# Performance work log

Hardware: AMD Instinct MI355X
Metric: run time of the kernel (lower is better)

Reference implementation:

```python
import jax, jax.numpy as jnp
import numpy as np

D, E, DFF, TOPK = 768, 4, 1024, 2


def setup_inputs() -> dict:
    key = jax.random.key(0)
    ks = jax.random.split(key, 6)
    s = 0.02  # init scale for weights
    return {
        "input_ids": jax.random.normal(ks[0], (8, 2048, D), dtype=jnp.float32),
        "W": jax.random.normal(ks[1], (D, D), dtype=jnp.float32) * s,
        "b": jnp.zeros((D,), dtype=jnp.float32),
        "Wg": jax.random.normal(ks[2], (D, E), dtype=jnp.float32) * s,
        "bg": jnp.zeros((E,), dtype=jnp.float32),
        "W1": jax.random.normal(ks[3], (E, D, DFF), dtype=jnp.float32) * s,
        "b1": jnp.zeros((E, DFF), dtype=jnp.float32),
        "W2": jax.random.normal(ks[4], (E, DFF, D), dtype=jnp.float32) * s,
        "b2": jnp.zeros((E, D), dtype=jnp.float32),
    }


def reference(input_ids, W, b, Wg, bg, W1, b1, W2, b2):
    B, S, _ = input_ids.shape
    # Dense projection feeding the MoE layer
    h = jnp.einsum("bsd,de->bse", input_ids, W) + b          # [B,S,D]
    t = h.reshape(-1, D)                                      # [T,D] tokens

    # Token-choice router: softmax over experts, top-2, renormalized gates
    logits = t @ Wg + bg                                      # [T,E]
    probs = jax.nn.softmax(logits, axis=-1)
    vals, idx = jax.lax.top_k(probs, TOPK)                    # [T,K]
    gates = vals / jnp.sum(vals, axis=-1, keepdims=True)
    # Dense combine weights [T,E]: zero for non-selected experts
    comb = jnp.sum(jax.nn.one_hot(idx, E, dtype=t.dtype) * gates[..., None], axis=1)

    # Expert FFNs (E small -> compute all experts, weighted combine)
    pre = jnp.einsum("td,edf->etf", t, W1) + b1[:, None, :]   # [E,T,DFF]
    y_e = jnp.einsum("etf,efd->etd", jax.nn.gelu(pre), W2) + b2[:, None, :]
    out = jnp.einsum("te,etd->td", comb, y_e)                 # [T,D]
    return out.reshape(B, S, D)
```

## Files before the change

kernel.cpp:

```cpp
#include <hip/hip_runtime.h>

#define DIM 768
#define NEXP 4
#define DFF_ 1024
#define CAP 16384

typedef __attribute__((ext_vector_type(4))) float f32x4;
typedef __attribute__((ext_vector_type(8))) short s16x8;

__device__ __forceinline__ unsigned short f32_to_bf16(float f) {
  unsigned int u = __float_as_uint(f);
  unsigned int r = (u + 0x7FFFu + ((u >> 16) & 1u)) >> 16;
  return (unsigned short)r;
}
__device__ __forceinline__ float bf16_to_f32(unsigned short u) {
  return __uint_as_float(((unsigned int)u) << 16);
}

__global__ void transpose_bf16_kernel(const float* __restrict__ in,
                                      unsigned short* __restrict__ out,
                                      int R, int C, int ldo, int zOut) {
  __shared__ float tile[32][33];
  const int bx = blockIdx.x, by = blockIdx.y, bz = blockIdx.z;
  in  += (size_t)bz * R * C;
  out += (size_t)bz * zOut;
  const int tx = threadIdx.x, ty = threadIdx.y;
#pragma unroll
  for (int i = 0; i < 4; i++) {
    int r = by * 32 + ty + i * 8;
    int c = bx * 32 + tx;
    tile[ty + i * 8][tx] = in[(size_t)r * C + c];
  }
  __syncthreads();
#pragma unroll
  for (int i = 0; i < 4; i++) {
    int oc = bx * 32 + ty + i * 8;
    int orow = by * 32 + tx;
    out[(size_t)oc * ldo + orow] = f32_to_bf16(tile[tx][ty + i * 8]);
  }
}

__global__ void wfg_kernel(const float* __restrict__ W, const float* __restrict__ Wg,
                           const float* __restrict__ b, const float* __restrict__ bg,
                           float* __restrict__ wfg, float* __restrict__ bgp) {
  int gid = blockIdx.x * 256 + threadIdx.x;
  if (gid < DIM * NEXP) {
    int k = gid >> 2, e = gid & 3;
    const float* wr = W + (size_t)k * DIM;
    float acc = 0.f;
    for (int d = 0; d < DIM; d++) acc += wr[d] * Wg[d * NEXP + e];
    wfg[gid] = acc;
  } else if (gid < DIM * NEXP + NEXP) {
    int e = gid - DIM * NEXP;
    float acc = bg[e];
    for (int d = 0; d < DIM; d++) acc += b[d] * Wg[d * NEXP + e];
    bgp[e] = acc;
  }
}

__global__ void router_kernel(const float* __restrict__ x, const float* __restrict__ wfg,
                              const float* __restrict__ bgp,
                              int2* __restrict__ rte, float2* __restrict__ rtg,
                              unsigned short* __restrict__ xbf) {
  __shared__ float wfgS[DIM * NEXP];
  const int tid = threadIdx.x;
  for (int i = tid; i < DIM * NEXP; i += 256) wfgS[i] = wfg[i];
  __syncthreads();
  const int w = tid >> 6, lane = tid & 63;
  const size_t t = (size_t)blockIdx.x * 4 + w;
  const float* xr = x + t * DIM;
  unsigned short* xbr = xbf + t * DIM;
  float a0 = 0.f, a1 = 0.f, a2 = 0.f, a3 = 0.f;
#pragma unroll
  for (int i = 0; i < 6; i++) {
    int k = i * 128 + lane * 2;
    float2 xv = *(const float2*)(xr + k);
    ushort2 pk;
    pk.x = f32_to_bf16(xv.x);
    pk.y = f32_to_bf16(xv.y);
    *(ushort2*)(xbr + k) = pk;
    a0 += xv.x * wfgS[k * 4 + 0] + xv.y * wfgS[k * 4 + 4];
    a1 += xv.x * wfgS[k * 4 + 1] + xv.y * wfgS[k * 4 + 5];
    a2 += xv.x * wfgS[k * 4 + 2] + xv.y * wfgS[k * 4 + 6];
    a3 += xv.x * wfgS[k * 4 + 3] + xv.y * wfgS[k * 4 + 7];
  }
#pragma unroll
  for (int off = 32; off > 0; off >>= 1) {
    a0 += __shfl_xor(a0, off);
    a1 += __shfl_xor(a1, off);
    a2 += __shfl_xor(a2, off);
    a3 += __shfl_xor(a3, off);
  }
  if (lane == 0) {
    float l[NEXP] = {a0 + bgp[0], a1 + bgp[1], a2 + bgp[2], a3 + bgp[3]};
    float m = fmaxf(fmaxf(l[0], l[1]), fmaxf(l[2], l[3]));
    float p[NEXP]; float s = 0.f;
#pragma unroll
    for (int e = 0; e < NEXP; e++) { p[e] = expf(l[e] - m); s += p[e]; }
#pragma unroll
    for (int e = 0; e < NEXP; e++) p[e] /= s;
    int i1 = 0;
#pragma unroll
    for (int e = 1; e < NEXP; e++) if (p[e] > p[i1]) i1 = e;
    int i2 = -1;
#pragma unroll
    for (int e = 0; e < NEXP; e++) { if (e == i1) continue; if (i2 < 0 || p[e] > p[i2]) i2 = e; }
    float denom = p[i1] + p[i2];
    rte[t] = make_int2(i1, i2);
    rtg[t] = make_float2(p[i1] / denom, p[i2] / denom);
  }
}

__global__ void assign_kernel(const int2* __restrict__ rte, const float2* __restrict__ rtg,
                              int* __restrict__ cnt, int* __restrict__ idx_tok,
                              float* __restrict__ gate_sel, int2* __restrict__ tok_slot) {
  __shared__ int hist[NEXP];
  __shared__ int base[NEXP];
  const int tid = threadIdx.x;
  if (tid < NEXP) hist[tid] = 0;
  __syncthreads();
  const int t = blockIdx.x * 256 + tid;
  int2 e = rte[t];
  float2 g = rtg[t];
  int r1 = atomicAdd(&hist[e.x], 1);
  int r2 = atomicAdd(&hist[e.y], 1);
  __syncthreads();
  if (tid < NEXP) base[tid] = atomicAdd(&cnt[tid], hist[tid]);
  __syncthreads();
  int s1 = base[e.x] + r1, s2 = base[e.y] + r2;
  idx_tok[e.x * CAP + s1] = t;  gate_sel[e.x * CAP + s1] = g.x;
  idx_tok[e.y * CAP + s2] = t;  gate_sel[e.y * CAP + s2] = g.y;
  tok_slot[t] = make_int2((e.x << 14) | s1, (e.y << 14) | s2);
}

__global__ void combine_kernel(const unsigned short* __restrict__ y,
                               const int2* __restrict__ tok_slot,
                               const float2* __restrict__ rtg,
                               const int* __restrict__ cnts,
                               const float* __restrict__ b2,
                               float* __restrict__ out) {
  __shared__ float b2S[NEXP * DIM];
  const int tid = threadIdx.x;
  for (int i = tid; i < NEXP * DIM; i += 256) b2S[i] = b2[i];
  const int t0 = (cnts[0] + 127) >> 7, t1 = (cnts[1] + 127) >> 7, t2 = (cnts[2] + 127) >> 7;
  const int rb[NEXP] = {0, t0 * 128, (t0 + t1) * 128, (t0 + t1 + t2) * 128};
  __syncthreads();
  const int w = tid >> 6, lane = tid & 63;
  const size_t t = (size_t)blockIdx.x * 4 + w;
  int2 v = tok_slot[t];
  float2 cg = rtg[t];
  const int e1 = v.x >> 14, s1 = v.x & (CAP - 1);
  const int e2 = v.y >> 14, s2 = v.y & (CAP - 1);
  const unsigned short* y1 = y + (size_t)(rb[e1] + s1) * DIM;
  const unsigned short* y2 = y + (size_t)(rb[e2] + s2) * DIM;
  float* op = out + t * DIM;
  const float* bp1 = b2S + e1 * DIM;
  const float* bp2 = b2S + e2 * DIM;
#pragma unroll
  for (int k = 0; k < 12; k++) {
    int n = k * 64 + lane;
    op[n] = bf16_to_f32(y1[n]) + bf16_to_f32(y2[n]) + cg.x * bp1[n] + cg.y * bp2[n];
  }
}

template <int MODE, int CH>
__launch_bounds__(256)
__global__ void gemm_kernel(const unsigned short* __restrict__ A, const int lda,
                            const unsigned short* __restrict__ Bt, const int ldb,
                            const int K, const int N,
                            const float* __restrict__ bias,
                            const int* __restrict__ idx_tok,
                            const float* __restrict__ gate_sel,
                            const int* __restrict__ cnts,
                            unsigned short* __restrict__ outB, const int ldo) {
  const int lin = blockIdx.y * gridDim.x + blockIdx.x;
  const int nT = gridDim.x;
  const int xcd = lin & 7, t8 = lin >> 3;
  int bn = 0, bm0 = 0;
  int bmLoc = 0, cnt = 1 << 30, segBase = 0, gRow0 = 0;

  if constexpr (MODE == 0) {
    const int perXcd = gridDim.y >> 3;
    const int mi = t8 % CH;
    const int rest = t8 / CH;
    bn = rest % nT;
    const int mc = rest / nT;
    bm0 = (xcd * perXcd + mc * CH + mi) * 128;
  } else {
    const int c0 = cnts[0], c1 = cnts[1], c2 = cnts[2], c3 = cnts[3];
    const int t0 = (c0 + 127) >> 7, t1 = (c1 + 127) >> 7,
              t2 = (c2 + 127) >> 7, t3 = (c3 + 127) >> 7;
    const int p1 = t0, p2 = p1 + t1, p3 = p2 + t2, tot = p3 + t3;
    const int perXcd = (tot + 7) >> 3;
    bn = t8 % nT;
    const int mloc = t8 / nT;
    if (mloc >= perXcd) return;
    const int mIdx = xcd * perXcd + mloc;
    if (mIdx >= tot) return;
    const int seg = (mIdx >= p2) ? ((mIdx >= p3) ? 3 : 2) : ((mIdx >= p1) ? 1 : 0);
    const int pre = (seg == 3) ? p3 : (seg == 2) ? p2 : (seg == 1) ? p1 : 0;
    bmLoc = (mIdx - pre) * 128;
    segBase = seg * CAP;
    gRow0 = mIdx * 128;
    cnt = (seg == 3) ? c3 : (seg == 2) ? c2 : (seg == 1) ? c1 : c0;
    Bt += (size_t)seg * N * ldb;
    if constexpr (MODE == 1) bias += (size_t)seg * N;
  }

  __shared__ unsigned short As[2][128 * 32];
  __shared__ unsigned short Bs[2][128 * 32];
  __shared__ int idxS[128];
  __shared__ float gateS[128];

  const int tid = threadIdx.x;
  const int w = tid >> 6;
  const int lane = tid & 63;

  if constexpr (MODE == 1) {
    if (tid < 128) {
      int r = bmLoc + tid;
      int cl = (r < cnt) ? r : bmLoc;
      idxS[tid] = idx_tok[segBase + cl];
      gateS[tid] = gate_sel[segBase + cl];
    }
    __syncthreads();
  }

  const int r0 = tid >> 2, r1 = 64 + r0;
  const int gq = (tid & 3) ^ (r0 & 3);
  const unsigned short *aP0, *aP1;
  if constexpr (MODE == 0) {
    aP0 = A + (size_t)(bm0 + r0) * lda + gq * 8;
    aP1 = A + (size_t)(bm0 + r1) * lda + gq * 8;
  } else if constexpr (MODE == 1) {
    aP0 = A + (size_t)idxS[r0] * lda + gq * 8;
    aP1 = A + (size_t)idxS[r1] * lda + gq * 8;
  } else {
    aP0 = A + (size_t)(gRow0 + r0) * lda + gq * 8;
    aP1 = A + (size_t)(gRow0 + r1) * lda + gq * 8;
  }
  const unsigned short* bP0 = Bt + (size_t)(bn * 128 + r0) * ldb + gq * 8;
  const unsigned short* bP1 = Bt + (size_t)(bn * 128 + r1) * ldb + gq * 8;

#define ISSUE(bufi, kk)                                                                        \
  {                                                                                            \
    char* la0 = (char*)As[bufi] + w * 1024;                                                    \
    char* la1 = (char*)As[bufi] + 4096 + w * 1024;                                             \
    char* lb0 = (char*)Bs[bufi] + w * 1024;                                                    \
    char* lb1 = (char*)Bs[bufi] + 4096 + w * 1024;                                             \
    __builtin_amdgcn_global_load_lds((const __attribute__((address_space(1))) void*)(aP0 + (kk)), \
                                     (__attribute__((address_space(3))) void*)la0, 16, 0, 0);  \
    __builtin_amdgcn_global_load_lds((const __attribute__((address_space(1))) void*)(aP1 + (kk)), \
                                     (__attribute__((address_space(3))) void*)la1, 16, 0, 0);  \
    __builtin_amdgcn_global_load_lds((const __attribute__((address_space(1))) void*)(bP0 + (kk)), \
                                     (__attribute__((address_space(3))) void*)lb0, 16, 0, 0);  \
    __builtin_amdgcn_global_load_lds((const __attribute__((address_space(1))) void*)(bP1 + (kk)), \
                                     (__attribute__((address_space(3))) void*)lb1, 16, 0, 0);  \
  }

  f32x4 acc[4][4];
#pragma unroll
  for (int i = 0; i < 4; i++)
#pragma unroll
    for (int j = 0; j < 4; j++) acc[i][j] = (f32x4){0.f, 0.f, 0.f, 0.f};

  const int quad = lane >> 4;
  const int m16 = lane & 15;
  const int wm = (w & 1) * 64;
  const int wn = (w >> 1) * 64;
  const int sw = (quad ^ (m16 & 3)) * 16;

  ISSUE(0, 0);
  int buf = 0;
  for (int k0 = 0; k0 < K; k0 += 32) {
    __syncthreads();
    if (k0 + 32 < K) ISSUE(buf ^ 1, k0 + 32);
    const char* Ab = (const char*)As[buf];
    const char* Bb = (const char*)Bs[buf];
    s16x8 af[4], bf4[4];
#pragma unroll
    for (int i = 0; i < 4; i++)
      af[i] = *(const s16x8*)(Ab + (wm + i * 16 + m16) * 64 + sw);
#pragma unroll
    for (int j = 0; j < 4; j++)
      bf4[j] = *(const s16x8*)(Bb + (wn + j * 16 + m16) * 64 + sw);
#pragma unroll
    for (int i = 0; i < 4; i++)
#pragma unroll
      for (int j = 0; j < 4; j++)
        acc[i][j] = __builtin_amdgcn_mfma_f32_16x16x32_bf16(af[i], bf4[j], acc[i][j], 0, 0, 0);
    buf ^= 1;
  }
#undef ISSUE

#pragma unroll
  for (int i = 0; i < 4; i++) {
    const int rloc = wm + i * 16 + quad * 4;
#pragma unroll
    for (int j = 0; j < 4; j++) {
      const int col = bn * 128 + wn + j * 16 + m16;
      if constexpr (MODE == 0) {
        float bv = bias[col];
#pragma unroll
        for (int r = 0; r < 4; r++)
          outB[(size_t)(bm0 + rloc + r) * ldo + col] = f32_to_bf16(acc[i][j][r] + bv);
      } else if constexpr (MODE == 1) {
        float bv = bias[col];
#pragma unroll
        for (int r = 0; r < 4; r++) {
          if (bmLoc + rloc + r < cnt) {
            float v = acc[i][j][r] + bv;
            float t3 = v + 0.044715f * v * v * v;
            float e2 = exp2f(t3 * 2.302208206984525f);
            float rc = __builtin_amdgcn_rcpf(1.0f + e2);
            float g = v - v * rc;
            outB[(size_t)(gRow0 + rloc + r) * ldo + col] = f32_to_bf16(g * gateS[rloc + r]);
          }
        }
      } else {
#pragma unroll
        for (int r = 0; r < 4; r++) {
          if (bmLoc + rloc + r < cnt)
            outB[(size_t)(gRow0 + rloc + r) * ldo + col] = f32_to_bf16(acc[i][j][r]);
        }
      }
    }
  }
}

extern "C" void kernel_launch(void* const* d_in, const int* in_sizes, int n_in,
                              void* d_out, int out_size, void* d_ws, size_t ws_size,
                              hipStream_t stream) {
  (void)in_sizes; (void)n_in; (void)out_size; (void)ws_size;
  const float* x  = (const float*)d_in[0];
  const float* W  = (const float*)d_in[1];
  const float* b  = (const float*)d_in[2];
  const float* Wg = (const float*)d_in[3];
  const float* bg = (const float*)d_in[4];
  const float* W1 = (const float*)d_in[5];
  const float* b1 = (const float*)d_in[6];
  const float* W2 = (const float*)d_in[7];
  const float* b2 = (const float*)d_in[8];
  float* out = (float*)d_out;
  char* ws = (char*)d_ws;

  unsigned short* tbf  = (unsigned short*)(ws + 0);
  unsigned short* w1t  = (unsigned short*)(ws + 25165824);
  unsigned short* w2t  = (unsigned short*)(ws + 31457280);
  float* wfg           = (float*)(ws + 37748736);
  float* bgp           = (float*)(ws + 37761024);
  int2*  rte           = (int2*)(ws + 37761280);
  float2* rtg          = (float2*)(ws + 37892352);
  int*   cnt           = (int*)(ws + 38023424);
  int*   idx_tok       = (int*)(ws + 38023680);
  float* gate_sel      = (float*)(ws + 38285824);
  int2*  tok_slot      = (int2*)(ws + 38547968);
  unsigned short* g    = (unsigned short*)(ws + 38679040);
  unsigned short* xbf  = (unsigned short*)(ws + 38679040);
  unsigned short* wt   = (unsigned short*)(ws + 63844864);
  unsigned short* y    = (unsigned short*)(ws + 106574336);

  hipMemsetAsync(cnt, 0, NEXP * sizeof(int), stream);
  transpose_bf16_kernel<<<dim3(24, 24, 1), dim3(32, 8), 0, stream>>>(W, wt, 768, 768, 768, 589824);
  transpose_bf16_kernel<<<dim3(32, 24, 4), dim3(32, 8), 0, stream>>>(W1, w1t, 768, 1024, 768, 786432);
  transpose_bf16_kernel<<<dim3(24, 32, 4), dim3(32, 8), 0, stream>>>(W2, w2t, 1024, 768, 1024, 786432);
  wfg_kernel<<<13, 256, 0, stream>>>(W, Wg, b, bg, wfg, bgp);
  router_kernel<<<4096, 256, 0, stream>>>(x, wfg, bgp, rte, rtg, xbf);
  assign_kernel<<<64, 256, 0, stream>>>(rte, rtg, cnt, idx_tok, gate_sel, tok_slot);

  gemm_kernel<0, 8><<<dim3(6, 128), 256, 0, stream>>>(
      xbf, 768, wt, 768, 768, 768, b, nullptr, nullptr, nullptr, tbf, 768);
  gemm_kernel<1, 8><<<dim3(8, 264), 256, 0, stream>>>(
      tbf, 768, w1t, 768, 768, 1024, b1, idx_tok, gate_sel, cnt, g, 1024);
  gemm_kernel<2, 8><<<dim3(6, 264), 256, 0, stream>>>(
      g, 1024, w2t, 1024, 1024, 768, nullptr, nullptr, nullptr, cnt, y, 768);
  combine_kernel<<<4096, 256, 0, stream>>>(y, tok_slot, rtg, cnt, b2, out);
}
```

Measured before the change: 403.8 us.

## Switch GEMMs to 256x256 tiles with 8 waves and ping-pong phased pipeline

Replaces the 128x128, 4-wave, K=32 double-buffered GEMM with a 256x256 tile using 512 threads, K=64 stages split into halves, and a four-phase schedule. The phases interleave LDS fragment loads, async global-to-LDS staging and MFMA bursts under barriers and setprio. Expert segment padding moves to 256 rows, so the combine offsets and the y workspace offset change to match. The aim is more data reuse per tile and better overlap of memory with MFMA. In exchange it adds padding waste per expert, needs more LDS and registers, and gives fewer blocks for load balance.

```diff
diff --git a/kernel.cpp b/kernel.cpp
--- a/kernel.cpp
+++ b/kernel.cpp
@@ -142,8 +142,8 @@
   __shared__ float b2S[NEXP * DIM];
   const int tid = threadIdx.x;
   for (int i = tid; i < NEXP * DIM; i += 256) b2S[i] = b2[i];
-  const int t0 = (cnts[0] + 127) >> 7, t1 = (cnts[1] + 127) >> 7, t2 = (cnts[2] + 127) >> 7;
-  const int rb[NEXP] = {0, t0 * 128, (t0 + t1) * 128, (t0 + t1 + t2) * 128};
+  const int t0 = (cnts[0] + 255) >> 8, t1 = (cnts[1] + 255) >> 8, t2 = (cnts[2] + 255) >> 8;
+  const int rb[NEXP] = {0, t0 * 256, (t0 + t1) * 256, (t0 + t1 + t2) * 256};
   __syncthreads();
   const int w = tid >> 6, lane = tid & 63;
   const size_t t = (size_t)blockIdx.x * 4 + w;
@@ -163,33 +163,33 @@
   }
 }
 
-template <int MODE, int CH>
-__launch_bounds__(256)
+template <int MODE, int KT>
+__launch_bounds__(512, 2)
 __global__ void gemm_kernel(const unsigned short* __restrict__ A, const int lda,
                             const unsigned short* __restrict__ Bt, const int ldb,
-                            const int K, const int N,
+                            const int N,
                             const float* __restrict__ bias,
                             const int* __restrict__ idx_tok,
                             const float* __restrict__ gate_sel,
                             const int* __restrict__ cnts,
                             unsigned short* __restrict__ outB, const int ldo) {
-  const int lin = blockIdx.y * gridDim.x + blockIdx.x;
-  const int nT = gridDim.x;
-  const int xcd = lin & 7, t8 = lin >> 3;
-  int bn = 0, bm0 = 0;
-  int bmLoc = 0, cnt = 1 << 30, segBase = 0, gRow0 = 0;
+  int bn = 0, bm0 = 0, bmLoc = 0, cnt = 1 << 30, segBase = 0, gRow0 = 0;
 
   if constexpr (MODE == 0) {
+    const int lin = blockIdx.y * gridDim.x + blockIdx.x;
+    const int xcd = lin & 7, t8 = lin >> 3;
+    const int nT = gridDim.x;
+    bn = t8 % nT;
+    const int mc = t8 / nT;
     const int perXcd = gridDim.y >> 3;
-    const int mi = t8 % CH;
-    const int rest = t8 / CH;
-    bn = rest % nT;
-    const int mc = rest / nT;
-    bm0 = (xcd * perXcd + mc * CH + mi) * 128;
+    bm0 = (xcd * perXcd + mc) * 256;
   } else {
+    const int lin = blockIdx.y * gridDim.x + blockIdx.x;
+    const int nT = gridDim.x;
+    const int xcd = lin & 7, t8 = lin >> 3;
     const int c0 = cnts[0], c1 = cnts[1], c2 = cnts[2], c3 = cnts[3];
-    const int t0 = (c0 + 127) >> 7, t1 = (c1 + 127) >> 7,
-              t2 = (c2 + 127) >> 7, t3 = (c3 + 127) >> 7;
+    const int t0 = (c0 + 255) >> 8, t1 = (c1 + 255) >> 8,
+              t2 = (c2 + 255) >> 8, t3 = (c3 + 255) >> 8;
     const int p1 = t0, p2 = p1 + t1, p3 = p2 + t2, tot = p3 + t3;
     const int perXcd = (tot + 7) >> 3;
     bn = t8 % nT;
@@ -199,25 +199,25 @@
     if (mIdx >= tot) return;
     const int seg = (mIdx >= p2) ? ((mIdx >= p3) ? 3 : 2) : ((mIdx >= p1) ? 1 : 0);
     const int pre = (seg == 3) ? p3 : (seg == 2) ? p2 : (seg == 1) ? p1 : 0;
-    bmLoc = (mIdx - pre) * 128;
+    bmLoc = (mIdx - pre) * 256;
     segBase = seg * CAP;
-    gRow0 = mIdx * 128;
+    gRow0 = mIdx * 256;
     cnt = (seg == 3) ? c3 : (seg == 2) ? c2 : (seg == 1) ? c1 : c0;
     Bt += (size_t)seg * N * ldb;
     if constexpr (MODE == 1) bias += (size_t)seg * N;
   }
 
-  __shared__ unsigned short As[2][128 * 32];
-  __shared__ unsigned short Bs[2][128 * 32];
-  __shared__ int idxS[128];
-  __shared__ float gateS[128];
+  __shared__ unsigned short As[2][2][128 * 64];
+  __shared__ unsigned short Bs[2][2][128 * 64];
+  __shared__ int idxS[256];
+  __shared__ float gateS[256];
 
   const int tid = threadIdx.x;
-  const int w = tid >> 6;
+  const int w8 = tid >> 6;
   const int lane = tid & 63;
 
   if constexpr (MODE == 1) {
-    if (tid < 128) {
+    if (tid < 256) {
       int r = bmLoc + tid;
       int cl = (r < cnt) ? r : bmLoc;
       idxS[tid] = idx_tok[segBase + cl];
@@ -226,102 +226,171 @@
     __syncthreads();
   }
 
-  const int r0 = tid >> 2, r1 = 64 + r0;
-  const int gq = (tid & 3) ^ (r0 & 3);
-  const unsigned short *aP0, *aP1;
-  if constexpr (MODE == 0) {
-    aP0 = A + (size_t)(bm0 + r0) * lda + gq * 8;
-    aP1 = A + (size_t)(bm0 + r1) * lda + gq * 8;
-  } else if constexpr (MODE == 1) {
-    aP0 = A + (size_t)idxS[r0] * lda + gq * 8;
-    aP1 = A + (size_t)idxS[r1] * lda + gq * 8;
-  } else {
-    aP0 = A + (size_t)(gRow0 + r0) * lda + gq * 8;
-    aP1 = A + (size_t)(gRow0 + r1) * lda + gq * 8;
-  }
-  const unsigned short* bP0 = Bt + (size_t)(bn * 128 + r0) * ldb + gq * 8;
-  const unsigned short* bP1 = Bt + (size_t)(bn * 128 + r1) * ldb + gq * 8;
-
-#define ISSUE(bufi, kk)                                                                        \
-  {                                                                                            \
-    char* la0 = (char*)As[bufi] + w * 1024;                                                    \
-    char* la1 = (char*)As[bufi] + 4096 + w * 1024;                                             \
-    char* lb0 = (char*)Bs[bufi] + w * 1024;                                                    \
-    char* lb1 = (char*)Bs[bufi] + 4096 + w * 1024;                                             \
-    __builtin_amdgcn_global_load_lds((const __attribute__((address_space(1))) void*)(aP0 + (kk)), \
-                                     (__attribute__((address_space(3))) void*)la0, 16, 0, 0);  \
-    __builtin_amdgcn_global_load_lds((const __attribute__((address_space(1))) void*)(aP1 + (kk)), \
-                                     (__attribute__((address_space(3))) void*)la1, 16, 0, 0);  \
-    __builtin_amdgcn_global_load_lds((const __attribute__((address_space(1))) void*)(bP0 + (kk)), \
-                                     (__attribute__((address_space(3))) void*)lb0, 16, 0, 0);  \
-    __builtin_amdgcn_global_load_lds((const __attribute__((address_space(1))) void*)(bP1 + (kk)), \
-                                     (__attribute__((address_space(3))) void*)lb1, 16, 0, 0);  \
-  }
-
-  f32x4 acc[4][4];
-#pragma unroll
-  for (int i = 0; i < 4; i++)
-#pragma unroll
-    for (int j = 0; j < 4; j++) acc[i][j] = (f32x4){0.f, 0.f, 0.f, 0.f};
-
-  const int quad = lane >> 4;
-  const int m16 = lane & 15;
-  const int wm = (w & 1) * 64;
-  const int wn = (w >> 1) * 64;
-  const int sw = (quad ^ (m16 & 3)) * 16;
-
-  ISSUE(0, 0);
-  int buf = 0;
-  for (int k0 = 0; k0 < K; k0 += 32) {
-    __syncthreads();
-    if (k0 + 32 < K) ISSUE(buf ^ 1, k0 + 32);
-    const char* Ab = (const char*)As[buf];
-    const char* Bb = (const char*)Bs[buf];
-    s16x8 af[4], bf4[4];
-#pragma unroll
-    for (int i = 0; i < 4; i++)
-      af[i] = *(const s16x8*)(Ab + (wm + i * 16 + m16) * 64 + sw);
-#pragma unroll
-    for (int j = 0; j < 4; j++)
-      bf4[j] = *(const s16x8*)(Bb + (wn + j * 16 + m16) * 64 + sw);
-#pragma unroll
-    for (int i = 0; i < 4; i++)
-#pragma unroll
-      for (int j = 0; j < 4; j++)
-        acc[i][j] = __builtin_amdgcn_mfma_f32_16x16x32_bf16(af[i], bf4[j], acc[i][j], 0, 0, 0);
-    buf ^= 1;
-  }
-#undef ISSUE
-
-#pragma unroll
-  for (int i = 0; i < 4; i++) {
-    const int rloc = wm + i * 16 + quad * 4;
-#pragma unroll
-    for (int j = 0; j < 4; j++) {
-      const int col = bn * 128 + wn + j * 16 + m16;
-      if constexpr (MODE == 0) {
-        float bv = bias[col];
-#pragma unroll
-        for (int r = 0; r < 4; r++)
-          outB[(size_t)(bm0 + rloc + r) * ldo + col] = f32_to_bf16(acc[i][j][r] + bv);
-      } else if constexpr (MODE == 1) {
-        float bv = bias[col];
-#pragma unroll
-        for (int r = 0; r < 4; r++) {
-          if (bmLoc + rloc + r < cnt) {
-            float v = acc[i][j][r] + bv;
-            float t3 = v + 0.044715f * v * v * v;
-            float e2 = exp2f(t3 * 2.302208206984525f);
-            float rc = __builtin_amdgcn_rcpf(1.0f + e2);
-            float g = v - v * rc;
-            outB[(size_t)(gRow0 + rloc + r) * ldo + col] = f32_to_bf16(g * gateS[rloc + r]);
+  const int srow = lane >> 3;
+  const int sslot = (lane & 7) ^ srow;
+  const unsigned short* aP[2][2];
+  const unsigned short* bP[2][2];
+#pragma unroll
+  for (int h = 0; h < 2; h++)
+#pragma unroll
+    for (int i = 0; i < 2; i++) {
+      const int rr = h * 128 + i * 64 + w8 * 8 + srow;
+      size_t arow;
+      if constexpr (MODE == 0) arow = (size_t)(bm0 + rr);
+      else if constexpr (MODE == 1) arow = (size_t)idxS[rr];
+      else arow = (size_t)(gRow0 + rr);
+      aP[h][i] = A + arow * lda + sslot * 8;
+      bP[h][i] = Bt + (size_t)(bn * 256 + rr) * ldb + sslot * 8;
+    }
+
+  const int wr = w8 >> 2, wc = w8 & 3;
+  const int m16 = lane & 15, q4 = lane >> 4;
+  const int rs = m16 & 7;
+  const int aBase = (wr * 64 + m16) * 128;
+  const int bBase = (wc * 32 + m16) * 128;
+  const int s0 = (q4 ^ rs) * 16;
+  const int s1 = ((4 + q4) ^ rs) * 16;
+
+  f32x4 acc[4][4][2];
+#pragma unroll
+  for (int a_ = 0; a_ < 4; a_++)
+#pragma unroll
+    for (int b_ = 0; b_ < 4; b_++)
+#pragma unroll
+      for (int c_ = 0; c_ < 2; c_++) acc[a_][b_][c_] = (f32x4){0.f, 0.f, 0.f, 0.f};
+  s16x8 aF[4][2], bF[2][2];
+
+#define BAR()                              \
+  {                                        \
+    asm volatile("" ::: "memory");         \
+    __builtin_amdgcn_s_barrier();          \
+    asm volatile("" ::: "memory");         \
+  }
+#define STAGE_A(bufi, half, kOff)                                                          \
+  {                                                                                        \
+    char* dA_ = (char*)&As[bufi][half][0] + w8 * 1024;                                     \
+    __builtin_amdgcn_global_load_lds(                                                      \
+        (const __attribute__((address_space(1))) void*)(aP[half][0] + (kOff)),             \
+        (__attribute__((address_space(3))) void*)(dA_), 16, 0, 0);                         \
+    __builtin_amdgcn_global_load_lds(                                                      \
+        (const __attribute__((address_space(1))) void*)(aP[half][1] + (kOff)),             \
+        (__attribute__((address_space(3))) void*)(dA_ + 8192), 16, 0, 0);                  \
+  }
+#define STAGE_B(bufi, half, kOff)                                                          \
+  {                                                                                        \
+    char* dB_ = (char*)&Bs[bufi][half][0] + w8 * 1024;                                     \
+    __builtin_amdgcn_global_load_lds(                                                      \
+        (const __attribute__((address_space(1))) void*)(bP[half][0] + (kOff)),             \
+        (__attribute__((address_space(3))) void*)(dB_), 16, 0, 0);                         \
+    __builtin_amdgcn_global_load_lds(                                                      \
+        (const __attribute__((address_space(1))) void*)(bP[half][1] + (kOff)),             \
+        (__attribute__((address_space(3))) void*)(dB_ + 8192), 16, 0, 0);                  \
+  }
+#define LOAD_A(bufc, qm)                                                 \
+  {                                                                      \
+    const char* Ah_ = (const char*)&As[bufc][qm][0];                     \
+    _Pragma("unroll") for (int fm_ = 0; fm_ < 4; fm_++) {                \
+      aF[fm_][0] = *(const s16x8*)(Ah_ + aBase + fm_ * 2048 + s0);       \
+      aF[fm_][1] = *(const s16x8*)(Ah_ + aBase + fm_ * 2048 + s1);       \
+    }                                                                    \
+  }
+#define LOAD_B(bufc, qn)                                                 \
+  {                                                                      \
+    const char* Bh_ = (const char*)&Bs[bufc][qn][0];                     \
+    _Pragma("unroll") for (int fn_ = 0; fn_ < 2; fn_++) {                \
+      bF[fn_][0] = *(const s16x8*)(Bh_ + bBase + fn_ * 2048 + s0);       \
+      bF[fn_][1] = *(const s16x8*)(Bh_ + bBase + fn_ * 2048 + s1);       \
+    }                                                                    \
+  }
+#define MFMA_PH(qi)                                                            \
+  {                                                                            \
+    __builtin_amdgcn_s_setprio(1);                                             \
+    _Pragma("unroll") for (int fm_ = 0; fm_ < 4; fm_++)                        \
+    _Pragma("unroll") for (int fn_ = 0; fn_ < 2; fn_++) {                      \
+      acc[qi][fm_][fn_] = __builtin_amdgcn_mfma_f32_16x16x32_bf16(             \
+          aF[fm_][0], bF[fn_][0], acc[qi][fm_][fn_], 0, 0, 0);                 \
+      acc[qi][fm_][fn_] = __builtin_amdgcn_mfma_f32_16x16x32_bf16(             \
+          aF[fm_][1], bF[fn_][1], acc[qi][fm_][fn_], 0, 0, 0);                 \
+    }                                                                          \
+    __builtin_amdgcn_s_setprio(0);                                             \
+  }
+#define KTILE_BODY(bufc, uu_, DO_S1, DO_S2, VMC4)                        \
+  {                                                                      \
+    const int kN1_ = ((uu_) + 1) * 64, kN2_ = ((uu_) + 2) * 64;          \
+    LOAD_A(bufc, 0); LOAD_B(bufc, 0);                                    \
+    if (DO_S1) STAGE_B((bufc) ^ 1, 0, kN1_);                             \
+    BAR(); MFMA_PH(0); BAR();                                            \
+    LOAD_B(bufc, 1);                                                     \
+    if (DO_S1) STAGE_A((bufc) ^ 1, 1, kN1_);                             \
+    BAR(); MFMA_PH(1); BAR();                                            \
+    LOAD_A(bufc, 1);                                                     \
+    if (DO_S2) STAGE_A((bufc), 0, kN2_);                                 \
+    BAR(); MFMA_PH(3); BAR();                                            \
+    LOAD_B(bufc, 0);                                                     \
+    if (DO_S2) STAGE_B((bufc), 1, kN2_);                                 \
+    if (VMC4) { asm volatile("s_waitcnt vmcnt(4)" ::: "memory"); }       \
+    else      { asm volatile("s_waitcnt vmcnt(0)" ::: "memory"); }       \
+    BAR(); MFMA_PH(2); BAR();                                            \
+  }
+
+  STAGE_A(0, 0, 0); STAGE_A(0, 1, 0);
+  STAGE_B(0, 0, 0); STAGE_B(0, 1, 0);
+  STAGE_A(1, 0, 64); STAGE_B(1, 1, 64);
+  asm volatile("s_waitcnt vmcnt(4)" ::: "memory");
+  BAR();
+
+  static_assert(KT >= 4 && (KT & 1) == 0, "KT must be even, >= 4");
+#pragma unroll 1
+  for (int uu = 0; uu < (KT - 2) / 2; uu++) {
+    KTILE_BODY(0, 2 * uu, 1, 1, 1);
+    KTILE_BODY(1, 2 * uu + 1, 1, 1, 1);
+  }
+  KTILE_BODY(0, KT - 2, 1, 0, 0);
+  KTILE_BODY(1, KT - 1, 0, 0, 0);
+
+#undef KTILE_BODY
+#undef MFMA_PH
+#undef LOAD_B
+#undef LOAD_A
+#undef STAGE_B
+#undef STAGE_A
+#undef BAR
+
+#pragma unroll
+  for (int qi = 0; qi < 4; qi++) {
+    const int qm = qi >> 1, qn = qi & 1;
+#pragma unroll
+    for (int fm = 0; fm < 4; fm++) {
+      const int r0 = qm * 128 + wr * 64 + fm * 16 + q4 * 4;
+#pragma unroll
+      for (int fn = 0; fn < 2; fn++) {
+        const int col = bn * 256 + qn * 128 + wc * 32 + fn * 16 + m16;
+        if constexpr (MODE == 0) {
+          const float bv = bias[col];
+#pragma unroll
+          for (int r = 0; r < 4; r++)
+            outB[(size_t)(bm0 + r0 + r) * ldo + col] = f32_to_bf16(acc[qi][fm][fn][r] + bv);
+        } else if constexpr (MODE == 1) {
+          const float bv = bias[col];
+#pragma unroll
+          for (int r = 0; r < 4; r++) {
+            const int ro = r0 + r;
+            if (bmLoc + ro < cnt) {
+              float v = acc[qi][fm][fn][r] + bv;
+              float t3 = v + 0.044715f * v * v * v;
+              float e2 = exp2f(t3 * 2.302208206984525f);
+              float rc = __builtin_amdgcn_rcpf(1.0f + e2);
+              float gl = v - v * rc;
+              outB[(size_t)(gRow0 + ro) * ldo + col] = f32_to_bf16(gl * gateS[ro]);
+            }
           }
-        }
-      } else {
-#pragma unroll
-        for (int r = 0; r < 4; r++) {
-          if (bmLoc + rloc + r < cnt)
-            outB[(size_t)(gRow0 + rloc + r) * ldo + col] = f32_to_bf16(acc[i][j][r]);
+        } else {
+#pragma unroll
+          for (int r = 0; r < 4; r++) {
+            const int ro = r0 + r;
+            if (bmLoc + ro < cnt)
+              outB[(size_t)(gRow0 + ro) * ldo + col] = f32_to_bf16(acc[qi][fm][fn][r]);
+          }
         }
       }
     }
@@ -358,7 +427,7 @@
   unsigned short* g    = (unsigned short*)(ws + 38679040);
   unsigned short* xbf  = (unsigned short*)(ws + 38679040);
   unsigned short* wt   = (unsigned short*)(ws + 63844864);
-  unsigned short* y    = (unsigned short*)(ws + 106574336);
+  unsigned short* y    = (unsigned short*)(ws + 107885056);
 
   hipMemsetAsync(cnt, 0, NEXP * sizeof(int), stream);
   transpose_bf16_kernel<<<dim3(24, 24, 1), dim3(32, 8), 0, stream>>>(W, wt, 768, 768, 768, 589824);
@@ -368,11 +437,11 @@
   router_kernel<<<4096, 256, 0, stream>>>(x, wfg, bgp, rte, rtg, xbf);
   assign_kernel<<<64, 256, 0, stream>>>(rte, rtg, cnt, idx_tok, gate_sel, tok_slot);
 
-  gemm_kernel<0, 8><<<dim3(6, 128), 256, 0, stream>>>(
-      xbf, 768, wt, 768, 768, 768, b, nullptr, nullptr, nullptr, tbf, 768);
-  gemm_kernel<1, 8><<<dim3(8, 264), 256, 0, stream>>>(
-      tbf, 768, w1t, 768, 768, 1024, b1, idx_tok, gate_sel, cnt, g, 1024);
-  gemm_kernel<2, 8><<<dim3(6, 264), 256, 0, stream>>>(
-      g, 1024, w2t, 1024, 1024, 768, nullptr, nullptr, nullptr, cnt, y, 768);
+  gemm_kernel<0, 12><<<dim3(3, 64), 512, 0, stream>>>(
+      xbf, 768, wt, 768, 768, b, nullptr, nullptr, nullptr, tbf, 768);
+  gemm_kernel<1, 12><<<dim3(4, 136), 512, 0, stream>>>(
+      tbf, 768, w1t, 768, 1024, b1, idx_tok, gate_sel, cnt, g, 1024);
+  gemm_kernel<2, 16><<<dim3(3, 136), 512, 0, stream>>>(
+      g, 1024, w2t, 1024, 768, nullptr, nullptr, nullptr, cnt, y, 768);
   combine_kernel<<<4096, 256, 0, stream>>>(y, tok_slot, rtg, cnt, b2, out);
 }
```

New measurement: 451.1 us. 11.7% more time.

## Triple-buffer GEMM LDS pipeline with explicit waitcnt and inline ds_read

Applied to the files above, without the earlier changes.

Changes the bf16 MFMA GEMM main loop from a double-buffered to a triple-buffered LDS pipeline with two tiles in flight. It uses explicit vmcnt waits, split barriers, hand-written ds_read_b128 with immediate offsets, and setprio around the MFMA block. K is now a compile-time tile count template parameter, and launch bounds request 3 waves per SIMD. The goal is to hide global-load latency better and cut address arithmetic, at the cost of more LDS per block, a second barrier per step, and fragile asm-based scheduling.

```diff
diff --git a/kernel.cpp b/kernel.cpp
--- a/kernel.cpp
+++ b/kernel.cpp
@@ -15,6 +15,9 @@
 }
 __device__ __forceinline__ float bf16_to_f32(unsigned short u) {
   return __uint_as_float(((unsigned int)u) << 16);
+}
+__device__ __forceinline__ unsigned lds_off(const void* p) {
+  return (unsigned)(unsigned long long)(__attribute__((address_space(3))) const void*)p;
 }
 
 __global__ void transpose_bf16_kernel(const float* __restrict__ in,
@@ -163,11 +166,11 @@
   }
 }
 
-template <int MODE, int CH>
-__launch_bounds__(256)
+template <int MODE, int CH, int NT>
+__launch_bounds__(256, 3)
 __global__ void gemm_kernel(const unsigned short* __restrict__ A, const int lda,
                             const unsigned short* __restrict__ Bt, const int ldb,
-                            const int K, const int N,
+                            const int N,
                             const float* __restrict__ bias,
                             const int* __restrict__ idx_tok,
                             const float* __restrict__ gate_sel,
@@ -207,8 +210,8 @@
     if constexpr (MODE == 1) bias += (size_t)seg * N;
   }
 
-  __shared__ unsigned short As[2][128 * 32];
-  __shared__ unsigned short Bs[2][128 * 32];
+  __shared__ unsigned short As[3][128 * 32];
+  __shared__ unsigned short Bs[3][128 * 32];
   __shared__ int idxS[128];
   __shared__ float gateS[128];
 
@@ -242,56 +245,87 @@
   const unsigned short* bP0 = Bt + (size_t)(bn * 128 + r0) * ldb + gq * 8;
   const unsigned short* bP1 = Bt + (size_t)(bn * 128 + r1) * ldb + gq * 8;
 
-#define ISSUE(bufi, kk)                                                                        \
-  {                                                                                            \
-    char* la0 = (char*)As[bufi] + w * 1024;                                                    \
-    char* la1 = (char*)As[bufi] + 4096 + w * 1024;                                             \
-    char* lb0 = (char*)Bs[bufi] + w * 1024;                                                    \
-    char* lb1 = (char*)Bs[bufi] + 4096 + w * 1024;                                             \
-    __builtin_amdgcn_global_load_lds((const __attribute__((address_space(1))) void*)(aP0 + (kk)), \
-                                     (__attribute__((address_space(3))) void*)la0, 16, 0, 0);  \
-    __builtin_amdgcn_global_load_lds((const __attribute__((address_space(1))) void*)(aP1 + (kk)), \
-                                     (__attribute__((address_space(3))) void*)la1, 16, 0, 0);  \
-    __builtin_amdgcn_global_load_lds((const __attribute__((address_space(1))) void*)(bP0 + (kk)), \
-                                     (__attribute__((address_space(3))) void*)lb0, 16, 0, 0);  \
-    __builtin_amdgcn_global_load_lds((const __attribute__((address_space(1))) void*)(bP1 + (kk)), \
-                                     (__attribute__((address_space(3))) void*)lb1, 16, 0, 0);  \
-  }
-
-  f32x4 acc[4][4];
-#pragma unroll
-  for (int i = 0; i < 4; i++)
-#pragma unroll
-    for (int j = 0; j < 4; j++) acc[i][j] = (f32x4){0.f, 0.f, 0.f, 0.f};
-
   const int quad = lane >> 4;
   const int m16 = lane & 15;
   const int wm = (w & 1) * 64;
   const int wn = (w >> 1) * 64;
   const int sw = (quad ^ (m16 & 3)) * 16;
 
+  const unsigned aBase0 = lds_off(&As[0][0]);
+  const unsigned bBase0 = lds_off(&Bs[0][0]);
+  const unsigned aRd = (unsigned)((wm + m16) * 64 + sw);
+  const unsigned bRd = (unsigned)((wn + m16) * 64 + sw);
+
+  f32x4 acc[4][4];
+#pragma unroll
+  for (int i = 0; i < 4; i++)
+#pragma unroll
+    for (int j = 0; j < 4; j++) acc[i][j] = (f32x4){0.f, 0.f, 0.f, 0.f};
+
+#define GLL(src, dst)                                                              \
+  __builtin_amdgcn_global_load_lds((const __attribute__((address_space(1))) void*)(src), \
+                                   (__attribute__((address_space(3))) void*)(dst), 16, 0, 0)
+#define ISSUE(off, kk)                                                   \
+  {                                                                      \
+    char* la0 = (char*)&As[0][0] + (off) + w * 1024;                     \
+    char* lb0 = (char*)&Bs[0][0] + (off) + w * 1024;                     \
+    GLL(aP0 + (kk), la0);                                                \
+    GLL(aP1 + (kk), la0 + 4096);                                         \
+    GLL(bP0 + (kk), lb0);                                                \
+    GLL(bP1 + (kk), lb0 + 4096);                                         \
+  }
+#define DSR(dst, addr, imm) \
+  asm volatile("ds_read_b128 %0, %1 offset:" #imm : "=v"(dst) : "v"(addr))
+#define KSTEP(GATE)                                                          \
+  {                                                                          \
+    asm volatile("s_waitcnt vmcnt(" #GATE ")" ::: "memory");                 \
+    __builtin_amdgcn_s_barrier();                                            \
+    asm volatile("" ::: "memory");                                           \
+    s16x8 af[4], bf4[4];                                                     \
+    const unsigned aAd = aBase0 + curOff + aRd;                              \
+    const unsigned bAd = bBase0 + curOff + bRd;                              \
+    DSR(af[0], aAd, 0);                                                      \
+    DSR(af[1], aAd, 1024);                                                   \
+    DSR(af[2], aAd, 2048);                                                   \
+    DSR(af[3], aAd, 3072);                                                   \
+    DSR(bf4[0], bAd, 0);                                                     \
+    DSR(bf4[1], bAd, 1024);                                                  \
+    DSR(bf4[2], bAd, 2048);                                                  \
+    DSR(bf4[3], bAd, 3072);                                                  \
+    asm volatile("s_waitcnt lgkmcnt(0)" ::: "memory");                       \
+    __builtin_amdgcn_sched_barrier(0);                                       \
+    __builtin_amdgcn_s_barrier();                                            \
+    asm volatile("" ::: "memory");                                           \
+    __builtin_amdgcn_s_setprio(1);                                           \
+    _Pragma("unroll") for (int i_ = 0; i_ < 4; i_++)                         \
+    _Pragma("unroll") for (int j_ = 0; j_ < 4; j_++)                         \
+      acc[i_][j_] = __builtin_amdgcn_mfma_f32_16x16x32_bf16(af[i_], bf4[j_], \
+                                                            acc[i_][j_], 0, 0, 0); \
+    __builtin_amdgcn_s_setprio(0);                                           \
+    curOff = (curOff == 16384u) ? 0u : curOff + 8192u;                       \
+  }
+
   ISSUE(0, 0);
-  int buf = 0;
-  for (int k0 = 0; k0 < K; k0 += 32) {
-    __syncthreads();
-    if (k0 + 32 < K) ISSUE(buf ^ 1, k0 + 32);
-    const char* Ab = (const char*)As[buf];
-    const char* Bb = (const char*)Bs[buf];
-    s16x8 af[4], bf4[4];
-#pragma unroll
-    for (int i = 0; i < 4; i++)
-      af[i] = *(const s16x8*)(Ab + (wm + i * 16 + m16) * 64 + sw);
-#pragma unroll
-    for (int j = 0; j < 4; j++)
-      bf4[j] = *(const s16x8*)(Bb + (wn + j * 16 + m16) * 64 + sw);
-#pragma unroll
-    for (int i = 0; i < 4; i++)
-#pragma unroll
-      for (int j = 0; j < 4; j++)
-        acc[i][j] = __builtin_amdgcn_mfma_f32_16x16x32_bf16(af[i], bf4[j], acc[i][j], 0, 0, 0);
-    buf ^= 1;
-  }
+  ISSUE(8192, 32);
+  unsigned curOff = 0;
+  unsigned stOff = 16384;
+  int kk = 64;
+
+  static_assert(NT >= 3, "NT must be >= 3");
+#pragma unroll 1
+  for (int i = 0; i < NT - 2; ++i) {
+    ISSUE(stOff, kk);
+    kk += 32;
+    stOff = (stOff == 16384u) ? 0u : stOff + 8192u;
+    KSTEP(8);
+  }
+  KSTEP(4);
+  KSTEP(0);
+
+#undef KSTEP
+#undef DSR
 #undef ISSUE
+#undef GLL
 
 #pragma unroll
   for (int i = 0; i < 4; i++) {
@@ -368,11 +402,11 @@
   router_kernel<<<4096, 256, 0, stream>>>(x, wfg, bgp, rte, rtg, xbf);
   assign_kernel<<<64, 256, 0, stream>>>(rte, rtg, cnt, idx_tok, gate_sel, tok_slot);
 
-  gemm_kernel<0, 8><<<dim3(6, 128), 256, 0, stream>>>(
-      xbf, 768, wt, 768, 768, 768, b, nullptr, nullptr, nullptr, tbf, 768);
-  gemm_kernel<1, 8><<<dim3(8, 264), 256, 0, stream>>>(
-      tbf, 768, w1t, 768, 768, 1024, b1, idx_tok, gate_sel, cnt, g, 1024);
-  gemm_kernel<2, 8><<<dim3(6, 264), 256, 0, stream>>>(
-      g, 1024, w2t, 1024, 1024, 768, nullptr, nullptr, nullptr, cnt, y, 768);
+  gemm_kernel<0, 8, 24><<<dim3(6, 128), 256, 0, stream>>>(
+      xbf, 768, wt, 768, 768, b, nullptr, nullptr, nullptr, tbf, 768);
+  gemm_kernel<1, 8, 24><<<dim3(8, 264), 256, 0, stream>>>(
+      tbf, 768, w1t, 768, 1024, b1, idx_tok, gate_sel, cnt, g, 1024);
+  gemm_kernel<2, 8, 32><<<dim3(6, 264), 256, 0, stream>>>(
+      g, 1024, w2t, 1024, 768, nullptr, nullptr, nullptr, cnt, y, 768);
   combine_kernel<<<4096, 256, 0, stream>>>(y, tok_slot, rtg, cnt, b2, out);
 }
```

Measured after the change: 397.6 us. No clear change (-1.5%).
